# Performance work log

Hardware: AMD Instinct MI355X
Metric: run time of the kernel (lower is better)

## Reference

```python
import jax, jax.numpy as jnp
import numpy as np

H = 2048      # hidden_size
NH = 16       # num_heads
HD = H // NH  # attention_head_size = 128
NEG_BIAS = -10000.0


def setup_inputs() -> dict:
    key = jax.random.key(0)
    k1, k2, k3, k4, k5 = jax.random.split(key, 5)
    B, S = 2, 2048
    hidden_states = jax.random.normal(k1, (B, S, H), dtype=jnp.float32)
    scale = 1.0 / np.sqrt(H)
    w_qkv = jax.random.normal(k2, (H, 3 * H), dtype=jnp.float32) * scale
    b_qkv = jax.random.normal(k3, (3 * H,), dtype=jnp.float32) * 0.01
    w_out = jax.random.normal(k4, (H, H), dtype=jnp.float32) * scale
    b_out = jax.random.normal(k5, (H,), dtype=jnp.float32) * 0.01
    return {"hidden_states": hidden_states, "w_qkv": w_qkv, "b_qkv": b_qkv,
            "w_out": w_out, "b_out": b_out}


def reference(hidden_states, w_qkv, b_qkv, w_out, b_out):
    B, S, _ = hidden_states.shape
    # fused QKV projection -> [B, S, 3H]
    qkv = hidden_states @ w_qkv + b_qkv
    # split heads with 3*head_dim per head, then chunk (matches torch code)
    qkv = qkv.reshape(B, S, NH, 3 * HD).transpose(0, 2, 1, 3)  # [B, NH, S, 3*HD]
    q, k, v = jnp.split(qkv, 3, axis=-1)                       # each [B, NH, S, HD]
    # scaled scores [B, NH, S, S]
    scores = jnp.einsum('bhqd,bhkd->bhqk', q, k) / np.sqrt(HD)
    causal = jnp.tril(jnp.ones((S, S), dtype=bool))
    scores = jnp.where(causal[None, None], scores, jnp.float32(NEG_BIAS))
    probs = jax.nn.softmax(scores, axis=-1)
    ctx = jnp.einsum('bhqk,bhkd->bhqd', probs, v)  # [B, NH, S, HD]
    ctx = ctx.transpose(0, 2, 1, 3).reshape(B, S, H)
    return ctx @ w_out + b_out
```

## Files before the change

### kernel.cpp

```cpp
#include <hip/hip_runtime.h>
#include <hip/hip_bf16.h>

typedef __bf16 bf16x8 __attribute__((ext_vector_type(8)));
typedef float  f32x4  __attribute__((ext_vector_type(4)));

constexpr int   Bb   = 2;
constexpr int   Slen = 2048;
constexpr int   Hdim = 2048;
constexpr int   NHn  = 16;
constexpr int   HDd  = 128;
constexpr int   LDP  = 136;
constexpr float QSCALE = 0.08838834764831845f;
constexpr float NEG    = -1e30f;

__device__ __forceinline__ void gld16(const __bf16* g, __bf16* l) {
    __builtin_amdgcn_global_load_lds(
        (__attribute__((address_space(1))) void*)(uintptr_t)(const void*)g,
        (__attribute__((address_space(3))) void*)l, 16, 0, 0);
}

__global__ __launch_bounds__(256) void cvt_bf16(const float* __restrict__ in,
                                                __bf16* __restrict__ out) {
    const size_t i = (size_t)(blockIdx.x * 256 + threadIdx.x) * 8;
    f32x4 a = *(const f32x4*)(in + i), b = *(const f32x4*)(in + i + 4);
    bf16x8 r;
    r[0] = (__bf16)a[0]; r[1] = (__bf16)a[1]; r[2] = (__bf16)a[2]; r[3] = (__bf16)a[3];
    r[4] = (__bf16)b[0]; r[5] = (__bf16)b[1]; r[6] = (__bf16)b[2]; r[7] = (__bf16)b[3];
    *(bf16x8*)(out + i) = r;
}

__global__ __launch_bounds__(256) void transpose_cvt(const float* __restrict__ in,
                                                     __bf16* __restrict__ out,
                                                     int R, int C) {
    __shared__ float t[64][65];
    const int c0 = blockIdx.x * 64, r0 = blockIdx.y * 64;
    const int tx = threadIdx.x & 63, ty = threadIdx.x >> 6;
#pragma unroll
    for (int i = 0; i < 16; ++i) {
        int r = i * 4 + ty;
        t[r][tx] = in[(size_t)(r0 + r) * C + c0 + tx];
    }
    __syncthreads();
#pragma unroll
    for (int i = 0; i < 16; ++i) {
        int r = i * 4 + ty;
        out[(size_t)(c0 + r) * R + r0 + tx] = (__bf16)t[tx][r];
    }
}

template <int MODE>
__global__ __launch_bounds__(256) void gemm_bt(
    const __bf16* __restrict__ A, const __bf16* __restrict__ Bt,
    const float* __restrict__ bias, int Kdim, int Ndim,
    float* __restrict__ Cout,
    __bf16* __restrict__ Qo, __bf16* __restrict__ Ko, __bf16* __restrict__ Vto) {
    __shared__ __bf16 As[128 * 32];
    __shared__ __bf16 Bs[128 * 32];
    const int tid = threadIdx.x;
    const int lane = tid & 63, wave = tid >> 6;
    const int quad = lane >> 4, l16 = lane & 15;
    const int wm = (wave >> 1) * 64, wn = (wave & 1) * 64;
    const int m0 = blockIdx.y * 128, n0 = blockIdx.x * 128;

    f32x4 acc[4][4] = {};

    for (int k0 = 0; k0 < Kdim; k0 += 32) {
        __syncthreads();
#pragma unroll
        for (int i = 0; i < 2; ++i) {
            int c = tid + i * 256;
            gld16(A  + (size_t)(m0 + (c >> 2)) * Kdim + k0 + (c & 3) * 8, As + c * 8);
            gld16(Bt + (size_t)(n0 + (c >> 2)) * Kdim + k0 + (c & 3) * 8, Bs + c * 8);
        }
        __syncthreads();
        bf16x8 af[4], bfr[4];
#pragma unroll
        for (int mi = 0; mi < 4; ++mi)
            af[mi] = *(const bf16x8*)(As + (wm + mi * 16 + l16) * 32 + quad * 8);
#pragma unroll
        for (int ni = 0; ni < 4; ++ni)
            bfr[ni] = *(const bf16x8*)(Bs + (wn + ni * 16 + l16) * 32 + quad * 8);
#pragma unroll
        for (int mi = 0; mi < 4; ++mi)
#pragma unroll
            for (int ni = 0; ni < 4; ++ni)
                acc[mi][ni] = __builtin_amdgcn_mfma_f32_16x16x32_bf16(
                    af[mi], bfr[ni], acc[mi][ni], 0, 0, 0);
    }

#pragma unroll
    for (int mi = 0; mi < 4; ++mi) {
#pragma unroll
        for (int r = 0; r < 4; ++r) {
            const int m = m0 + wm + mi * 16 + quad * 4 + r;
            const int b = m >> 11, s = m & 2047;
#pragma unroll
            for (int ni = 0; ni < 4; ++ni) {
                const int cc = n0 + wn + ni * 16 + l16;
                float val = acc[mi][ni][r] + bias[cc];
                if (MODE == 1) {
                    Cout[(size_t)m * Ndim + cc] = val;
                } else {
                    const int h = cc / 384;
                    const int rr = cc - h * 384;
                    const size_t hb = ((size_t)(b * NHn + h) * Slen + s);
                    if (rr < 128)
                        Qo[hb * HDd + rr] = (__bf16)(val * QSCALE);
                    else if (rr < 256)
                        Ko[hb * HDd + (rr - 128)] = (__bf16)val;
                    else
                        Vto[((size_t)(b * NHn + h) * HDd + (rr - 256)) * Slen + s] = (__bf16)val;
                }
            }
        }
    }
}

__global__ __launch_bounds__(256) void attn_k(const __bf16* __restrict__ Q,
                                              const __bf16* __restrict__ Kmat,
                                              const __bf16* __restrict__ Vt,
                                              __bf16* __restrict__ ctx) {
    __shared__ __bf16 Ks[128 * LDP];
    __shared__ __bf16 Vs[128 * LDP];
    const int tid = threadIdx.x, lane = tid & 63, wave = tid >> 6;
    const int quad = lane >> 4, l16 = lane & 15;
    const int bh = blockIdx.y;
    const int qt = gridDim.x - 1 - blockIdx.x;
    const int b = bh >> 4, h = bh & 15;
    const __bf16* Qb = Q    + (size_t)bh * Slen * HDd;
    const __bf16* Kb = Kmat + (size_t)bh * Slen * HDd;
    const __bf16* Vb = Vt   + (size_t)bh * HDd * Slen;
    const int q0 = qt * 64;
    const int qa = q0 + wave * 16 + l16;
    const int qc = q0 + wave * 16 + quad * 4;

    bf16x8 qf[4];
#pragma unroll
    for (int kk = 0; kk < 4; ++kk)
        qf[kk] = *(const bf16x8*)(Qb + (size_t)qa * HDd + kk * 32 + quad * 8);

    f32x4 accO[8] = {};
    float m_i[4] = {NEG, NEG, NEG, NEG};
    float l_i[4] = {0.f, 0.f, 0.f, 0.f};

    const int ktiles = (q0 + 63) / 128 + 1;
    for (int kt = 0; kt < ktiles; ++kt) {
        const int kb0 = kt * 128;
        __syncthreads();
#pragma unroll
        for (int i = 0; i < 8; ++i) {
            int c = tid + i * 256;
            *(bf16x8*)(Ks + (c >> 4) * LDP + (c & 15) * 8) =
                *(const bf16x8*)(Kb + (size_t)(kb0 + (c >> 4)) * HDd + (c & 15) * 8);
            *(bf16x8*)(Vs + (c >> 4) * LDP + (c & 15) * 8) =
                *(const bf16x8*)(Vb + (size_t)(c >> 4) * Slen + kb0 + (c & 15) * 8);
        }
        __syncthreads();

        f32x4 sc[8];
#pragma unroll
        for (int nk = 0; nk < 8; ++nk) {
            f32x4 z = {0.f, 0.f, 0.f, 0.f};
#pragma unroll
            for (int kk = 0; kk < 4; ++kk) {
                bf16x8 kf = *(const bf16x8*)(Ks + (nk * 16 + l16) * LDP + kk * 32 + quad * 8);
                z = __builtin_amdgcn_mfma_f32_16x16x32_bf16(qf[kk], kf, z, 0, 0, 0);
            }
            sc[nk] = z;
        }
        if (kt == ktiles - 1) {
#pragma unroll
            for (int nk = 0; nk < 8; ++nk) {
                const int kg = kb0 + nk * 16 + l16;
#pragma unroll
                for (int r = 0; r < 4; ++r)
                    if (kg > qc + r) sc[nk][r] = NEG;
            }
        }
#pragma unroll
        for (int r = 0; r < 4; ++r) {
            float mm = sc[0][r];
#pragma unroll
            for (int nk = 1; nk < 8; ++nk) mm = fmaxf(mm, sc[nk][r]);
            mm = fmaxf(mm, __shfl_xor(mm, 1));
            mm = fmaxf(mm, __shfl_xor(mm, 2));
            mm = fmaxf(mm, __shfl_xor(mm, 4));
            mm = fmaxf(mm, __shfl_xor(mm, 8));
            const float mnew = fmaxf(m_i[r], mm);
            const float alpha = __expf(m_i[r] - mnew);
            float ls = 0.f;
#pragma unroll
            for (int nk = 0; nk < 8; ++nk) {
                float p = __expf(sc[nk][r] - mnew);
                sc[nk][r] = p;
                ls += p;
            }
            ls += __shfl_xor(ls, 1);
            ls += __shfl_xor(ls, 2);
            ls += __shfl_xor(ls, 4);
            ls += __shfl_xor(ls, 8);
            l_i[r] = l_i[r] * alpha + ls;
            m_i[r] = mnew;
#pragma unroll
            for (int nd = 0; nd < 8; ++nd) accO[nd][r] *= alpha;
        }

        __syncthreads();
        __bf16* Ps = Ks + wave * 16 * LDP;
#pragma unroll
        for (int nk = 0; nk < 8; ++nk)
#pragma unroll
            for (int r = 0; r < 4; ++r)
                Ps[(quad * 4 + r) * LDP + nk * 16 + l16] = (__bf16)sc[nk][r];
        __syncthreads();

        bf16x8 pf[4];
#pragma unroll
        for (int kk = 0; kk < 4; ++kk)
            pf[kk] = *(const bf16x8*)(Ps + l16 * LDP + kk * 32 + quad * 8);
#pragma unroll
        for (int nd = 0; nd < 8; ++nd)
#pragma unroll
            for (int kk = 0; kk < 4; ++kk) {
                bf16x8 vf = *(const bf16x8*)(Vs + (nd * 16 + l16) * LDP + kk * 32 + quad * 8);
                accO[nd] = __builtin_amdgcn_mfma_f32_16x16x32_bf16(pf[kk], vf, accO[nd], 0, 0, 0);
            }
    }

#pragma unroll
    for (int nd = 0; nd < 8; ++nd)
#pragma unroll
        for (int r = 0; r < 4; ++r) {
            const int s = q0 + wave * 16 + quad * 4 + r;
            const int d = nd * 16 + l16;
            const float o = accO[nd][r] / fmaxf(l_i[r], 1e-20f);
            ctx[((size_t)b * Slen + s) * Hdim + h * HDd + d] = (__bf16)o;
        }
}

extern "C" void kernel_launch(void* const* d_in, const int* in_sizes, int n_in,
                              void* d_out, int out_size, void* d_ws, size_t ws_size,
                              hipStream_t stream) {
    const float* hs   = (const float*)d_in[0];
    const float* wqkv = (const float*)d_in[1];
    const float* bqkv = (const float*)d_in[2];
    const float* wout = (const float*)d_in[3];
    const float* bout = (const float*)d_in[4];
    float* out = (float*)d_out;

    __bf16* ws    = (__bf16*)d_ws;
    __bf16* wqkvT = ws;
    __bf16* woutT = wqkvT + (size_t)6144 * 2048;
    __bf16* Qs    = woutT + (size_t)2048 * 2048;
    __bf16* Kms   = Qs  + (size_t)Bb * NHn * Slen * HDd;
    __bf16* Vts   = Kms + (size_t)Bb * NHn * Slen * HDd;
    __bf16* ctx   = Vts + (size_t)Bb * NHn * Slen * HDd;
    __bf16* hsb   = ctx;

    cvt_bf16<<<(Bb * Slen * Hdim) / (256 * 8), 256, 0, stream>>>(hs, hsb);
    transpose_cvt<<<dim3(6144 / 64, 2048 / 64), 256, 0, stream>>>(wqkv, wqkvT, 2048, 6144);
    transpose_cvt<<<dim3(2048 / 64, 2048 / 64), 256, 0, stream>>>(wout, woutT, 2048, 2048);
    gemm_bt<0><<<dim3(6144 / 128, 4096 / 128), 256, 0, stream>>>(
        hsb, wqkvT, bqkv, Hdim, 3 * Hdim, nullptr, Qs, Kms, Vts);
    attn_k<<<dim3(Slen / 64, Bb * NHn), 256, 0, stream>>>(Qs, Kms, Vts, ctx);
    gemm_bt<1><<<dim3(2048 / 128, 4096 / 128), 256, 0, stream>>>(
        ctx, woutT, bout, Hdim, Hdim, out, nullptr, nullptr, nullptr);
}
```

Measured before the change: 499.9 us.

## Replace GEMM with 256x256-tile, 8-wave, double-buffered swizzled-LDS pipelined kernel

Both projection GEMMs move from a 128x128 tile with 4 waves and a single LDS buffer to a 256x256 tile with 8 waves, BK=64, and two LDS buffers. Global-to-LDS loads are split into quarter stages and interleaved with four MFMA phases using explicit vmcnt and lgkmcnt waits and barriers, with s_setprio raised around the MFMA blocks. The LDS layout is XOR-swizzled to avoid bank conflicts. This aims to hide load latency and raise arithmetic intensity, at the cost of 128KB of LDS, heavier register use, and fewer blocks for the smaller output GEMM.

New measurement: 486.5 us. 1.03x faster.

```diff
diff --git a/kernel.cpp b/kernel.cpp
--- a/kernel.cpp
+++ b/kernel.cpp
@@ -48,55 +48,124 @@
     }
 }
 
+
+#define BAR    __builtin_amdgcn_s_barrier()
+#define LGKM0  asm volatile("s_waitcnt lgkmcnt(0)" ::: "memory")
+#define VMC(n) asm volatile("s_waitcnt vmcnt(" #n ")" ::: "memory")
+
+#define STAGE(op, half, tt)                                                          \
+  do {                                                                               \
+    const int tt_ = (tt);                                                            \
+    if (tt_ < NT) {                                                                  \
+      __bf16* dst_ = lds + ((tt_ & 1) << 15) + ((op) << 14) + ((half) << 13);        \
+      const __bf16* src_ = (op) ? Bt : A;                                            \
+      const int rb_ = (op) ? n0 : m0;                                               \
+      const int k0_ = tt_ << 6;                                                      \
+      _Pragma("unroll")                                                              \
+      for (int i_ = 0; i_ < 2; ++i_) {                                               \
+        const int c_  = (i_ << 9) + tid;                                             \
+        const int rl_ = c_ >> 3;                                                     \
+        const int grow_ = rb_ + ((op) ? (((rl_ >> 5) << 6) + ((half) << 5) + (rl_ & 31)) \
+                                      : (((rl_ >> 6) << 7) + ((half) << 6) + (rl_ & 63))); \
+        const int gk_ = k0_ + (((c_ & 7) ^ (rl_ & 7)) << 3);                         \
+        gld16(src_ + (size_t)grow_ * Kdim + gk_, dst_ + (c_ << 3));                  \
+      }                                                                              \
+    }                                                                                \
+  } while (0)
+
+#define LDA(bufv, mh)                                                                \
+  do {                                                                               \
+    const __bf16* Ab_ = lds + ((bufv) << 15) + ((mh) << 13) + (wg << 12) + (l16 << 6); \
+    _Pragma("unroll")                                                                \
+    for (int q_ = 0; q_ < 4; ++q_)                                                   \
+      _Pragma("unroll")                                                              \
+      for (int kk_ = 0; kk_ < 2; ++kk_)                                              \
+        af[q_][kk_] = *(const bf16x8*)(Ab_ + (q_ << 10) +                            \
+                        ((((kk_ << 2) + quad) ^ (l16 & 7)) << 3));                   \
+  } while (0)
+
+#define LDB(bufv, nh)                                                                \
+  do {                                                                               \
+    const __bf16* Bb_ = lds + ((bufv) << 15) + 16384 + ((nh) << 13) + (gn << 11) + (l16 << 6); \
+    _Pragma("unroll")                                                                \
+    for (int q_ = 0; q_ < 2; ++q_)                                                   \
+      _Pragma("unroll")                                                              \
+      for (int kk_ = 0; kk_ < 2; ++kk_)                                              \
+        bfr[((nh) << 1) + q_][kk_] = *(const bf16x8*)(Bb_ + (q_ << 10) +             \
+                        ((((kk_ << 2) + quad) ^ (l16 & 7)) << 3));                   \
+  } while (0)
+
+#define MM(mh, nh)                                                                   \
+  do {                                                                               \
+    _Pragma("unroll")                                                                \
+    for (int q_ = 0; q_ < 4; ++q_)                                                   \
+      _Pragma("unroll")                                                              \
+      for (int n_ = 0; n_ < 2; ++n_)                                                 \
+        _Pragma("unroll")                                                            \
+        for (int kk_ = 0; kk_ < 2; ++kk_)                                            \
+          acc[((mh) << 2) + q_][((nh) << 1) + n_] =                                  \
+            __builtin_amdgcn_mfma_f32_16x16x32_bf16(                                 \
+              af[q_][kk_], bfr[((nh) << 1) + n_][kk_],                               \
+              acc[((mh) << 2) + q_][((nh) << 1) + n_], 0, 0, 0);                     \
+  } while (0)
+
 template <int MODE>
-__global__ __launch_bounds__(256) void gemm_bt(
+__global__ __launch_bounds__(512, 2) void gemm8(
     const __bf16* __restrict__ A, const __bf16* __restrict__ Bt,
     const float* __restrict__ bias, int Kdim, int Ndim,
     float* __restrict__ Cout,
     __bf16* __restrict__ Qo, __bf16* __restrict__ Ko, __bf16* __restrict__ Vto) {
-    __shared__ __bf16 As[128 * 32];
-    __shared__ __bf16 Bs[128 * 32];
-    const int tid = threadIdx.x;
+    __shared__ __bf16 lds[65536];
+    const int tid  = threadIdx.x;
     const int lane = tid & 63, wave = tid >> 6;
     const int quad = lane >> 4, l16 = lane & 15;
-    const int wm = (wave >> 1) * 64, wn = (wave & 1) * 64;
-    const int m0 = blockIdx.y * 128, n0 = blockIdx.x * 128;
-
-    f32x4 acc[4][4] = {};
-
-    for (int k0 = 0; k0 < Kdim; k0 += 32) {
-        __syncthreads();
-#pragma unroll
-        for (int i = 0; i < 2; ++i) {
-            int c = tid + i * 256;
-            gld16(A  + (size_t)(m0 + (c >> 2)) * Kdim + k0 + (c & 3) * 8, As + c * 8);
-            gld16(Bt + (size_t)(n0 + (c >> 2)) * Kdim + k0 + (c & 3) * 8, Bs + c * 8);
-        }
-        __syncthreads();
-        bf16x8 af[4], bfr[4];
-#pragma unroll
-        for (int mi = 0; mi < 4; ++mi)
-            af[mi] = *(const bf16x8*)(As + (wm + mi * 16 + l16) * 32 + quad * 8);
-#pragma unroll
-        for (int ni = 0; ni < 4; ++ni)
-            bfr[ni] = *(const bf16x8*)(Bs + (wn + ni * 16 + l16) * 32 + quad * 8);
-#pragma unroll
-        for (int mi = 0; mi < 4; ++mi)
-#pragma unroll
-            for (int ni = 0; ni < 4; ++ni)
-                acc[mi][ni] = __builtin_amdgcn_mfma_f32_16x16x32_bf16(
-                    af[mi], bfr[ni], acc[mi][ni], 0, 0, 0);
-    }
-
-#pragma unroll
-    for (int mi = 0; mi < 4; ++mi) {
+    const int wg = wave >> 2;
+    const int gn = wave & 3;
+    const int m0 = blockIdx.y * 256, n0 = blockIdx.x * 256;
+    const int NT = Kdim >> 6;
+
+    f32x4  acc[8][4] = {};
+    bf16x8 af[4][2];
+    bf16x8 bfr[4][2];
+
+    STAGE(0, 0, 0); STAGE(1, 0, 0); STAGE(1, 1, 0); STAGE(0, 1, 0);
+    STAGE(0, 0, 1); STAGE(1, 0, 1); STAGE(1, 1, 1);
+    VMC(6);
+    BAR;
+
+    for (int t = 0; t < NT; ++t) {
+        const int cb = t & 1;
+        LDA(cb, 0); LDB(cb, 0);
+        STAGE(0, 1, t + 1);
+        BAR; LGKM0;
+        __builtin_amdgcn_s_setprio(1); MM(0, 0); __builtin_amdgcn_s_setprio(0);
+        BAR;
+        LDB(cb, 1);
+        STAGE(0, 0, t + 2);
+        BAR; LGKM0;
+        __builtin_amdgcn_s_setprio(1); MM(0, 1); __builtin_amdgcn_s_setprio(0);
+        BAR;
+        LDA(cb, 1);
+        STAGE(1, 0, t + 2);
+        BAR; LGKM0;
+        __builtin_amdgcn_s_setprio(1); MM(1, 1); __builtin_amdgcn_s_setprio(0);
+        BAR;
+        STAGE(1, 1, t + 2);
+        if (t < NT - 2) { VMC(6); } else { VMC(0); }
+        BAR;
+        __builtin_amdgcn_s_setprio(1); MM(1, 0); __builtin_amdgcn_s_setprio(0);
+        BAR;
+    }
+
+#pragma unroll
+    for (int mi = 0; mi < 8; ++mi) {
 #pragma unroll
         for (int r = 0; r < 4; ++r) {
-            const int m = m0 + wm + mi * 16 + quad * 4 + r;
+            const int m = m0 + wg * 128 + (mi >> 2) * 64 + (mi & 3) * 16 + quad * 4 + r;
             const int b = m >> 11, s = m & 2047;
 #pragma unroll
             for (int ni = 0; ni < 4; ++ni) {
-                const int cc = n0 + wn + ni * 16 + l16;
+                const int cc = n0 + gn * 64 + (ni >> 1) * 32 + (ni & 1) * 16 + l16;
                 float val = acc[mi][ni][r] + bias[cc];
                 if (MODE == 1) {
                     Cout[(size_t)m * Ndim + cc] = val;
@@ -260,9 +329,9 @@
     cvt_bf16<<<(Bb * Slen * Hdim) / (256 * 8), 256, 0, stream>>>(hs, hsb);
     transpose_cvt<<<dim3(6144 / 64, 2048 / 64), 256, 0, stream>>>(wqkv, wqkvT, 2048, 6144);
     transpose_cvt<<<dim3(2048 / 64, 2048 / 64), 256, 0, stream>>>(wout, woutT, 2048, 2048);
-    gemm_bt<0><<<dim3(6144 / 128, 4096 / 128), 256, 0, stream>>>(
+    gemm8<0><<<dim3(6144 / 256, 4096 / 256), 512, 0, stream>>>(
         hsb, wqkvT, bqkv, Hdim, 3 * Hdim, nullptr, Qs, Kms, Vts);
     attn_k<<<dim3(Slen / 64, Bb * NHn), 256, 0, stream>>>(Qs, Kms, Vts, ctx);
-    gemm_bt<1><<<dim3(2048 / 128, 4096 / 128), 256, 0, stream>>>(
+    gemm8<1><<<dim3(2048 / 256, 4096 / 256), 512, 0, stream>>>(
         ctx, woutT, bout, Hdim, Hdim, out, nullptr, nullptr, nullptr);
 }
```
